# Performance work log

Measured on AMD Instinct MI355X. Metric: run time of the kernel, lower is better.

Reference implementation:

```python
import jax, jax.numpy as jnp
import numpy as np

B, N, DIM = 4, 1024, 512
DEPTH, HEADS, DH = 4, 8, 64
INNER = HEADS * DH  # 512
W = 32              # sqrt(N), FeedForward reshapes tokens to (W, W)
SCALE = DH ** -0.5  # used for BOTH spatial and spectral branches (as in source)
EPS_LN = 1e-5
EPS_BN = 1e-5


def setup_inputs() -> dict:
    key = jax.random.key(0)
    ks = jax.random.split(key, 16)
    L = DEPTH
    def rn(k, shape, s=0.02):
        return jax.random.normal(k, shape, jnp.float32) * s
    return {
        "x": jax.random.normal(ks[0], (B, N, DIM), jnp.float32),
        "ln1_w": jnp.ones((L, DIM), jnp.float32), "ln1_b": jnp.zeros((L, DIM), jnp.float32),
        "Wqkv": rn(ks[1], (L, DIM, 3 * INNER)),
        "Wout": rn(ks[2], (L, INNER, DIM)), "bout": jnp.zeros((L, DIM), jnp.float32),
        "sp_w": rn(ks[3], (L, HEADS, HEADS, 3, 3), 0.1), "sp_b": jnp.zeros((L, HEADS), jnp.float32),
        "Wqkv_spec": rn(ks[4], (L, N, 3 * N)),
        "spec_w": rn(ks[5], (L, 1, 1, 3, 3), 0.1), "spec_b": jnp.zeros((L, 1), jnp.float32),
        "ln2_w": jnp.ones((L, DIM), jnp.float32), "ln2_b": jnp.zeros((L, DIM), jnp.float32),
        "dw_w": rn(ks[6], (L, DIM, 1, 3, 3), 0.1), "dw_b": jnp.zeros((L, DIM), jnp.float32),
        "pw_w": rn(ks[7], (L, 256, DIM)), "pw_b": jnp.zeros((L, 256), jnp.float32),
        "bn_g": jnp.ones((L, 256), jnp.float32), "bn_b": jnp.zeros((L, 256), jnp.float32),
        "bn_m": jnp.zeros((L, 256), jnp.float32), "bn_v": jnp.ones((L, 256), jnp.float32),
        "c1_w": rn(ks[8], (L, 512, 256)), "c1_b": jnp.zeros((L, 512), jnp.float32),
        "c2_w": rn(ks[9], (L, DIM, 512)), "c2_b": jnp.zeros((L, DIM), jnp.float32),
    }


def _ln(x, w, b):
    mu = x.mean(-1, keepdims=True)
    var = x.var(-1, keepdims=True)  # biased, matching torch LayerNorm
    return (x - mu) * jax.lax.rsqrt(var + EPS_LN) * w + b


def _conv3x3(x, w, b, groups=1):
    y = jax.lax.conv_general_dilated(x, w, (1, 1), 'SAME',
                                     dimension_numbers=('NCHW', 'OIHW', 'NCHW'),
                                     feature_group_count=groups)
    return y + b[None, :, None, None]


def _block(x, p):
    (ln1w, ln1b, Wqkv, Wout, bout, spw, spb, Wqs, scw, scb,
     ln2w, ln2b, dww, dwb, pww, pwb, bng, bnb, bnm, bnv, c1w, c1b, c2w, c2b) = p
    b = x.shape[0]
    # --- spatial attention (PreNorm) ---
    h = _ln(x, ln1w, ln1b)
    q, k, v = jnp.split(h @ Wqkv, 3, axis=-1)
    split_heads = lambda t: t.reshape(b, N, HEADS, DH).transpose(0, 2, 1, 3)  # b h n d
    q, k, v = split_heads(q), split_heads(k), split_heads(v)
    attn = jax.nn.softmax(jnp.einsum('bhid,bhjd->bhij', q, k) * SCALE, axis=-1)
    attn = _conv3x3(attn, spw, spb)  # conv over the softmax map (heads as channels)
    out = jnp.einsum('bhij,bhjd->bhid', attn, v).transpose(0, 2, 1, 3).reshape(b, N, INNER)
    out = out @ Wout + bout  # (b, n, dim)
    # --- spectral attention on h^T (b, dim, n); v_spec is dead code in source ---
    xt = jnp.swapaxes(h, -1, -2)
    qs, ks_, _vs = jnp.split(xt @ Wqs, 3, axis=-1)  # each (b, dim, n)
    a = jax.nn.softmax(jnp.einsum('bin,bjn->bij', qs, ks_) * SCALE, axis=-1)
    a = _conv3x3(a[:, None], scw, scb)[:, 0]  # (b, dim, dim)
    x = x + jnp.einsum('bnd,bde->bne', out, a)  # residual add from Transformer loop
    # --- FeedForward (PreNorm), FF adds its own internal residual too ---
    h2 = _ln(x, ln2w, ln2b)
    img = h2.reshape(b, W, W, DIM).transpose(0, 3, 1, 2)  # 'b (w h) c -> b c w h'
    t = _conv3x3(img, dww, dwb, groups=DIM)               # depthwise 3x3
    t = jnp.einsum('oc,bchw->bohw', pww, t) + pwb[None, :, None, None]  # pointwise dim->256
    t = (t - bnm[None, :, None, None]) * jax.lax.rsqrt(bnv + EPS_BN)[None, :, None, None] \
        * bng[None, :, None, None] + bnb[None, :, None, None]           # BatchNorm2d (eval)
    t = jax.nn.gelu(jnp.einsum('oc,bchw->bohw', c1w, t) + c1b[None, :, None, None], approximate=False)
    t = jax.nn.gelu(jnp.einsum('oc,bchw->bohw', c2w, t) + c2b[None, :, None, None], approximate=False)
    ff = h2 + t.transpose(0, 2, 3, 1).reshape(b, N, DIM)  # FF internal residual
    return x + ff


def _forward(x, ln1_w, ln1_b, Wqkv, Wout, bout, sp_w, sp_b, Wqkv_spec, spec_w, spec_b,
             ln2_w, ln2_b, dw_w, dw_b, pw_w, pw_b, bn_g, bn_b, bn_m, bn_v,
             c1_w, c1_b, c2_w, c2_b):
    stacked = (ln1_w, ln1_b, Wqkv, Wout, bout, sp_w, sp_b, Wqkv_spec, spec_w, spec_b,
               ln2_w, ln2_b, dw_w, dw_b, pw_w, pw_b, bn_g, bn_b, bn_m, bn_v,
               c1_w, c1_b, c2_w, c2_b)
    for i in range(DEPTH):
        x = _block(x, tuple(a[i] for a in stacked))
    return x


def reference(x, ln1_w, ln1_b, Wqkv, Wout, bout, sp_w, sp_b, Wqkv_spec, spec_w, spec_b,
              ln2_w, ln2_b, dw_w, dw_b, pw_w, pw_b, bn_g, bn_b, bn_m, bn_v,
              c1_w, c1_b, c2_w, c2_b):
    return _forward(x, ln1_w, ln1_b, Wqkv, Wout, bout, sp_w, sp_b, Wqkv_spec, spec_w, spec_b,
                    ln2_w, ln2_b, dw_w, dw_b, pw_w, pw_b, bn_g, bn_b, bn_m, bn_v,
                    c1_w, c1_b, c2_w, c2_b)
```

## Files before the change

kernel.cpp:

```cpp
#include <hip/hip_runtime.h>
#include <hip/hip_bf16.h>

typedef __hip_bfloat16 bf16;
typedef __attribute__((ext_vector_type(8))) short bf16x8;
typedef __attribute__((ext_vector_type(4))) float f32x4;

__device__ __forceinline__ float b2f(bf16 v){ return __bfloat162float(v); }
__device__ __forceinline__ bf16 f2b(float v){ return __float2bfloat16(v); }
__device__ __forceinline__ float bits2f(unsigned u){ return __uint_as_float(u << 16); }
__device__ __forceinline__ unsigned short f2bits(float v){ bf16 t = __float2bfloat16(v); return *(unsigned short*)&t; }

__device__ __forceinline__ float gelu_f(float x){
  return 0.5f * x * (1.f + erff(x * 0.7071067811865475f));
}

__device__ __forceinline__ void gload_lds(const void* g, void* l){
  __builtin_amdgcn_global_load_lds((const __attribute__((address_space(1))) void*)g,
                                   (__attribute__((address_space(3))) void*)l, 16, 0, 0);
}

template<bool MAX>
__device__ __forceinline__ float block_reduce(float v){
  __shared__ float s[4];
  #pragma unroll
  for (int o = 32; o > 0; o >>= 1){
    float t = __shfl_down(v, o, 64);
    v = MAX ? fmaxf(v, t) : (v + t);
  }
  int lane = threadIdx.x & 63, w = threadIdx.x >> 6;
  __syncthreads();
  if (lane == 0) s[w] = v;
  __syncthreads();
  return MAX ? fmaxf(fmaxf(s[0], s[1]), fmaxf(s[2], s[3]))
             : (s[0] + s[1] + s[2] + s[3]);
}

__global__ void detect_k(const unsigned* __restrict__ x, int* __restrict__ flag){
  __shared__ int cnt[256];
  int tid = threadIdx.x;
  int c = 0;
  for (int i = tid; i < 4096; i += 256){
    unsigned h = x[i] & 0xffffu;
    int e = (int)((h >> 7) & 0xff);
    if (h == 0u || (e >= 100 && e <= 133)) c++;
  }
  cnt[tid] = c;
  __syncthreads();
  for (int o = 128; o > 0; o >>= 1){ if (tid < o) cnt[tid] += cnt[tid+o]; __syncthreads(); }
  if (tid == 0) *flag = (cnt[0] < 2048) ? 1 : 0;
}

__global__ __launch_bounds__(256) void cvt_x_k(const void* __restrict__ src,
                                               float* __restrict__ X,
                                               const int* __restrict__ flag){
  int p = blockIdx.x*256 + threadIdx.x;
  X[p] = (*flag) ? ((const float*)src)[p]
                 : __bfloat162float(((const bf16*)src)[p]);
}

struct WCvt21 { const void* src[21]; long long cum[22]; };

__global__ __launch_bounds__(256) void cvt_w_k(WCvt21 a, bf16* __restrict__ WB,
                                               long long total, const int* __restrict__ flag){
  long long i = (long long)blockIdx.x*256 + threadIdx.x;
  if (i >= total) return;
  int t = 0;
  while (a.cum[t+1] <= i) t++;
  long long e = i - a.cum[t];
  WB[i] = (*flag) ? __float2bfloat16(((const float*)a.src[t])[e])
                  : ((const bf16*)a.src[t])[e];
}

__global__ __launch_bounds__(256) void wtrans_k(const void* __restrict__ src, bf16* __restrict__ dst,
                                                int ld_src, int ldd, long long sSrc, long long sDst,
                                                const int* __restrict__ flag){
  __shared__ bf16 t[64][65];
  int z = blockIdx.z;
  int r0 = blockIdx.x*64, c0 = blockIdx.y*64;
  int lane = threadIdx.x & 63, quad = threadIdx.x >> 6;
  const float* sf = (const float*)src;
  const bf16* sb = (const bf16*)src;
  int fl = *flag;
  #pragma unroll
  for (int k = 0; k < 16; ++k){
    int r = quad*16 + k;
    long long idx = z*sSrc + (long long)(r0+r)*ld_src + c0 + lane;
    float v = fl ? sf[idx] : b2f(sb[idx]);
    t[r][lane] = f2b(v);
  }
  __syncthreads();
  #pragma unroll
  for (int k = 0; k < 16; ++k){
    int c = quad*16 + k;
    dst[z*sDst + (long long)(c0+c)*ldd + r0 + lane] = t[lane][c];
  }
}

__global__ void wprep_k(const bf16* __restrict__ spw, bf16* __restrict__ Wr){
  int l = blockIdx.x;
  for (int t = threadIdx.x; t < 1536; t += 256){
    int ho = t / 96, k = t - ho*96;
    float v = 0.f;
    if (ho < 8 && k < 72){
      int tap = k >> 3, hi = k & 7;
      v = b2f(spw[l*576 + ho*72 + hi*9 + tap]);
    }
    Wr[l*1536 + t] = f2b(v);
  }
}

__global__ __launch_bounds__(256) void store_out_k(const float* __restrict__ X,
                                                   void* __restrict__ out,
                                                   const int* __restrict__ flag){
  int p = blockIdx.x*256 + threadIdx.x;
  if (*flag) ((float*)out)[p] = X[p];
  else       ((bf16*)out)[p] = f2b(X[p]);
}

template<int MF, int NF, typename TC>
__global__ __launch_bounds__(256) void gmfma_k(
    int M, int N, int K,
    const bf16* __restrict__ A, int lda, long long sA, long long sA2,
    const bf16* __restrict__ Bt, int ldb, long long sB, long long sB2,
    TC* __restrict__ C, int ldc, long long sC, long long sC2,
    float alpha, int beta,
    const bf16* __restrict__ bias_n,
    const float* __restrict__ scale_n,
    const float* __restrict__ shift_n,
    const bf16* __restrict__ addF,
    int act)
{
  constexpr int BM = MF*32, BN = NF*32;
  constexpr int CHA = BM/16, CH = (BM+BN)/16;
  static_assert(CH % 4 == 0, "chunks must divide among 4 waves");
  __shared__ bf16 Asm[BM][32];
  __shared__ bf16 Bsm[BN][32];
  const int tid = threadIdx.x;
  const int lane = tid & 63, wid = tid >> 6;
  const int wm = wid >> 1, wn = wid & 1;
  const int m0 = blockIdx.y*BM, n0 = blockIdx.x*BN;
  const int z = blockIdx.z;
  const long long zl = z & 7, zh = z >> 3;
  const bf16* Ab = A + zl*sA + zh*sA2;
  const bf16* Bb = Bt + zl*sB + zh*sB2;
  TC* Cb = C + zl*sC + zh*sC2;
  const bf16* Fb = addF ? addF + zl*sC + zh*sC2 : nullptr;

  f32x4 acc[MF][NF];
  f32x4 zero = {0.f, 0.f, 0.f, 0.f};
  #pragma unroll
  for (int m = 0; m < MF; ++m)
    #pragma unroll
    for (int n = 0; n < NF; ++n) acc[m][n] = zero;

  const int rchunk = lane >> 2;
  const int kchunk = (lane & 3) * 8;
  const int row16 = lane & 15, kq = (lane >> 4) * 8;

  for (int k0 = 0; k0 < K; k0 += 32){
    #pragma unroll
    for (int cc = 0; cc < CH/4; ++cc){
      int c = wid + cc*4;
      if (c < CHA){
        int row = c*16 + rchunk;
        gload_lds(Ab + (long long)(m0+row)*lda + k0 + kchunk, &Asm[c*16][0]);
      } else {
        int row = (c-CHA)*16 + rchunk;
        gload_lds(Bb + (long long)(n0+row)*ldb + k0 + kchunk, &Bsm[(c-CHA)*16][0]);
      }
    }
    __syncthreads();
    bf16x8 af[MF], bfr[NF];
    #pragma unroll
    for (int m = 0; m < MF; ++m)
      af[m] = *(const bf16x8*)&Asm[wm*(MF*16) + m*16 + row16][kq];
    #pragma unroll
    for (int n = 0; n < NF; ++n)
      bfr[n] = *(const bf16x8*)&Bsm[wn*(NF*16) + n*16 + row16][kq];
    #pragma unroll
    for (int m = 0; m < MF; ++m)
      #pragma unroll
      for (int n = 0; n < NF; ++n)
        acc[m][n] = __builtin_amdgcn_mfma_f32_16x16x32_bf16(af[m], bfr[n], acc[m][n], 0, 0, 0);
    __syncthreads();
  }

  #pragma unroll
  for (int m = 0; m < MF; ++m){
    #pragma unroll
    for (int n = 0; n < NF; ++n){
      int gn = n0 + wn*(NF*16) + n*16 + (lane & 15);
      float bn_ = bias_n ? b2f(bias_n[gn]) : 0.f;
      float sc = scale_n ? scale_n[gn] : 1.f;
      float sh = shift_n ? shift_n[gn] : 0.f;
      #pragma unroll
      for (int r = 0; r < 4; ++r){
        int gm = m0 + wm*(MF*16) + m*16 + (lane >> 4)*4 + r;
        float v = acc[m][n][r] * alpha + bn_;
        v = v * sc + sh;
        if (act) v = gelu_f(v);
        long long idx = (long long)gm*ldc + gn;
        if (Fb) v += b2f(Fb[idx]);
        if (beta){
          float old;
          if constexpr (__is_same(TC, float)) old = Cb[idx]; else old = b2f(Cb[idx]);
          v += old;
        }
        if constexpr (__is_same(TC, float)) Cb[idx] = v; else Cb[idx] = f2b(v);
      }
    }
  }
}

template<int MF, int NF, typename TC>
static void gmfma_x(hipStream_t st, int z, int M, int N, int K,
                    const bf16* A, int lda, long long sA, long long sA2,
                    const bf16* Bt, int ldb, long long sB, long long sB2,
                    TC* C, int ldc, long long sC, long long sC2,
                    float alpha = 1.f, int beta = 0,
                    const bf16* bias_n = nullptr,
                    const float* scale_n = nullptr, const float* shift_n = nullptr,
                    const bf16* addF = nullptr, int act = 0)
{
  dim3 g(N/(NF*32), M/(MF*32), z);
  gmfma_k<MF,NF,TC><<<g, 256, 0, st>>>(M,N,K,A,lda,sA,sA2,Bt,ldb,sB,sB2,C,ldc,sC,sC2,
                                       alpha,beta,bias_n,scale_n,shift_n,addF,act);
}

template<int MF, int NF, typename TC>
static void gmfma(hipStream_t st, int z, int M, int N, int K,
                  const bf16* A, int lda, long long sA,
                  const bf16* Bt, int ldb, long long sB,
                  TC* C, int ldc, long long sC,
                  float alpha = 1.f, int beta = 0,
                  const bf16* bias_n = nullptr,
                  const float* scale_n = nullptr, const float* shift_n = nullptr,
                  const bf16* addF = nullptr, int act = 0)
{
  gmfma_x<MF,NF,TC>(st, z, M, N, K, A, lda, sA, 8*sA, Bt, ldb, sB, 8*sB,
                    C, ldc, sC, 8*sC, alpha, beta, bias_n, scale_n, shift_n, addF, act);
}

__global__ __launch_bounds__(256) void ln_k(const float* __restrict__ X, bf16* __restrict__ Y,
                                            const bf16* __restrict__ w, const bf16* __restrict__ b){
  long long row = blockIdx.x;
  const float* x = X + row*512;
  bf16* y = Y + row*512;
  int tid = threadIdx.x;
  float v0 = x[tid], v1 = x[tid+256];
  float mean = block_reduce<false>(v0+v1) * (1.f/512.f);
  float msq  = block_reduce<false>(v0*v0+v1*v1) * (1.f/512.f);
  float var = msq - mean*mean;
  float rs = rsqrtf(var + 1e-5f);
  y[tid]     = f2b((v0-mean)*rs*b2f(w[tid])     + b2f(b[tid]));
  y[tid+256] = f2b((v1-mean)*rs*b2f(w[tid+256]) + b2f(b[tid+256]));
}

__device__ __forceinline__ float ldf(const float* p){ return *p; }
__device__ __forceinline__ void stf(float* p, float v){ *p = v; }

__global__ __launch_bounds__(256) void softmax_k(float* __restrict__ data, int cols){
  long long row = blockIdx.x;
  float* p = data + row * (long long)cols;
  int tid = threadIdx.x;
  int per = cols >> 8;
  float v[4];
  float mx = -3.4e38f;
  for (int r = 0; r < per; ++r){ v[r] = p[tid + (r<<8)]; mx = fmaxf(mx, v[r]); }
  mx = block_reduce<true>(mx);
  float sum = 0.f;
  for (int r = 0; r < per; ++r){ v[r] = expf(v[r] - mx); sum += v[r]; }
  sum = block_reduce<false>(sum);
  float inv = 1.f / sum;
  for (int r = 0; r < per; ++r) p[tid + (r<<8)] = v[r] * inv;
}

__global__ __launch_bounds__(256) void smT_k(const bf16* __restrict__ Sp, bf16* __restrict__ Sx,
                                             long long bstride){
  __shared__ unsigned short sm[8][1032];
  __shared__ float redmx[4][8];
  __shared__ float redsum[4][8];
  int i = blockIdx.x;
  long long b = blockIdx.y;
  const bf16* src = Sp + b*bstride + (long long)i*1024;
  bf16* dst = Sx + b*bstride + (long long)i*8192;
  int tid = threadIdx.x;
  int lane = tid & 63, w = tid >> 6;
  int j0 = tid*4;

  float v[8][4];
  #pragma unroll
  for (int h = 0; h < 8; ++h){
    ushort4 u = *(const ushort4*)&src[h*1048576 + j0];
    v[h][0] = bits2f(u.x); v[h][1] = bits2f(u.y);
    v[h][2] = bits2f(u.z); v[h][3] = bits2f(u.w);
  }
  float mx[8];
  #pragma unroll
  for (int h = 0; h < 8; ++h){
    float m = fmaxf(fmaxf(v[h][0], v[h][1]), fmaxf(v[h][2], v[h][3]));
    #pragma unroll
    for (int o = 32; o > 0; o >>= 1) m = fmaxf(m, __shfl_xor(m, o, 64));
    if (lane == 0) redmx[w][h] = m;
    mx[h] = m;
  }
  __syncthreads();
  #pragma unroll
  for (int h = 0; h < 8; ++h)
    mx[h] = fmaxf(fmaxf(redmx[0][h], redmx[1][h]), fmaxf(redmx[2][h], redmx[3][h]));
  float inv[8];
  #pragma unroll
  for (int h = 0; h < 8; ++h){
    float s = 0.f;
    #pragma unroll
    for (int r = 0; r < 4; ++r){ v[h][r] = expf(v[h][r] - mx[h]); s += v[h][r]; }
    #pragma unroll
    for (int o = 32; o > 0; o >>= 1) s += __shfl_xor(s, o, 64);
    if (lane == 0) redsum[w][h] = s;
  }
  __syncthreads();
  #pragma unroll
  for (int h = 0; h < 8; ++h)
    inv[h] = 1.f / (redsum[0][h] + redsum[1][h] + redsum[2][h] + redsum[3][h]);
  #pragma unroll
  for (int h = 0; h < 8; ++h)
    #pragma unroll
    for (int r = 0; r < 4; ++r)
      sm[h][j0 + r] = f2bits(v[h][r] * inv[h]);
  __syncthreads();
  #pragma unroll
  for (int r = 0; r < 4; ++r){
    int j = j0 + r;
    bf16x8 o;
    #pragma unroll
    for (int h = 0; h < 8; ++h) o[h] = (short)sm[h][j];
    *(bf16x8*)&dst[(long long)j*8] = o;
  }
}

__global__ __launch_bounds__(256) void convmf_k(const bf16* __restrict__ Sx, bf16* __restrict__ Pout,
                                                const bf16* __restrict__ Wr, const bf16* __restrict__ bias,
                                                long long bstride){
  __shared__ bf16 tile[6][66][8];
  long long b = blockIdx.z;
  int i0 = blockIdx.y*4, j0 = blockIdx.x*64;
  int tid = threadIdx.x;
  const bf16* src = Sx + b*bstride;
  for (int t = tid; t < 396; t += 256){
    int row = t / 66, col = t - row*66;
    int gi = i0 + row - 1, gj = j0 + col - 1;
    bf16x8 val = {};
    if ((unsigned)gi < 1024u && (unsigned)gj < 1024u)
      val = *(const bf16x8*)&src[(long long)gi*8192 + gj*8];
    *(bf16x8*)&tile[row][col][0] = val;
  }
  int lane = tid & 63, wid = tid >> 6;
  int row16 = lane & 15, q = lane >> 4;
  bf16x8 bf0 = *(const bf16x8*)&Wr[row16*96 +  0 + q*8];
  bf16x8 bf1 = *(const bf16x8*)&Wr[row16*96 + 32 + q*8];
  bf16x8 bf2 = *(const bf16x8*)&Wr[row16*96 + 64 + q*8];
  __syncthreads();

  int ii = wid;
  f32x4 zero = {0.f,0.f,0.f,0.f};
  f32x4 acc[4] = {zero, zero, zero, zero};
  #pragma unroll
  for (int ks = 0; ks < 3; ++ks){
    int tap = ks*4 + q;
    int tcl = tap > 8 ? 0 : tap;
    int di = tcl / 3, dj = tcl - di*3;
    bf16x8 bsel = ks == 0 ? bf0 : (ks == 1 ? bf1 : bf2);
    #pragma unroll
    for (int mf = 0; mf < 4; ++mf){
      bf16x8 af = *(const bf16x8*)&tile[ii + di][mf*16 + row16 + dj][0];
      acc[mf] = __builtin_amdgcn_mfma_f32_16x16x32_bf16(af, bsel, acc[mf], 0, 0, 0);
    }
  }
  if (row16 < 8){
    float bv = b2f(bias[row16]);
    bf16* dst = Pout + b*bstride + (long long)row16*1048576 + (long long)(i0 + ii)*1024;
    #pragma unroll
    for (int mf = 0; mf < 4; ++mf){
      int j = j0 + mf*16 + q*4;
      ushort4 o;
      o.x = f2bits(acc[mf][0] + bv);
      o.y = f2bits(acc[mf][1] + bv);
      o.z = f2bits(acc[mf][2] + bv);
      o.w = f2bits(acc[mf][3] + bv);
      *(ushort4*)&dst[j] = o;
    }
  }
}

__global__ __launch_bounds__(256) void conv_spec_k(const float* __restrict__ in, bf16* __restrict__ out,
                                                   const bf16* __restrict__ w, const bf16* __restrict__ bias){
  __shared__ float ti[66][67];
  __shared__ bf16 toutT[64][65];
  int b = blockIdx.z;
  int i0 = blockIdx.y*64, j0 = blockIdx.x*64;
  int tid = threadIdx.x;
  const float* ib = in + (long long)b*262144;
  for (int t = tid; t < 66*66; t += 256){
    int r = t / 66, c = t - r*66;
    int gi = i0 + r - 1, gj = j0 + c - 1;
    float v = 0.f;
    if ((unsigned)gi < 512u && (unsigned)gj < 512u) v = ib[gi*512 + gj];
    ti[r][c] = v;
  }
  __syncthreads();
  float w9[9], bv = b2f(bias[0]);
  #pragma unroll
  for (int d = 0; d < 9; ++d) w9[d] = b2f(w[d]);
  int ii = tid & 63;
  #pragma unroll
  for (int q = 0; q < 16; ++q){
    int jj = (tid >> 6)*16 + q;
    float acc = bv;
    #pragma unroll
    for (int di = 0; di < 3; ++di)
      #pragma unroll
      for (int dj = 0; dj < 3; ++dj)
        acc += w9[di*3+dj] * ti[ii+di][jj+dj];
    toutT[jj][ii] = f2b(acc);
  }
  __syncthreads();
  #pragma unroll
  for (int q = 0; q < 16; ++q){
    int jj = (tid >> 6)*16 + q;
    out[(long long)b*262144 + (j0+jj)*512 + i0 + (tid & 63)] = toutT[jj][tid & 63];
  }
}

__global__ __launch_bounds__(256) void dwconv_k(const bf16* __restrict__ H2, bf16* __restrict__ T1,
                                                const bf16* __restrict__ w, const bf16* __restrict__ bias){
  int p = blockIdx.x*256 + threadIdx.x;
  int cp = p & 255;
  int n = (p >> 8) & 1023;
  int b = p >> 18;
  int c0 = cp*2;
  int wi = n >> 5, hg = n & 31;
  float a0 = b2f(bias[c0]), a1 = b2f(bias[c0+1]);
  #pragma unroll
  for (int di = 0; di < 3; ++di){
    int gw = wi + di - 1;
    if ((unsigned)gw >= 32u) continue;
    #pragma unroll
    for (int dj = 0; dj < 3; ++dj){
      int gh = hg + dj - 1;
      if ((unsigned)gh >= 32u) continue;
      unsigned hv = *(const unsigned*)&H2[((long long)b*1024 + (gw*32+gh))*512 + c0];
      float w0 = b2f(w[c0*9 + di*3 + dj]);
      float w1 = b2f(w[(c0+1)*9 + di*3 + dj]);
      a0 += w0 * bits2f(hv & 0xffffu);
      a1 += w1 * bits2f(hv >> 16);
    }
  }
  bf16 h0 = f2b(a0), h1 = f2b(a1);
  unsigned o = ((unsigned)*(unsigned short*)&h1 << 16) | (unsigned)*(unsigned short*)&h0;
  *(unsigned*)&T1[((long long)b*1024 + n)*512 + c0] = o;
}

__global__ void bnaff_all_k(const bf16* __restrict__ pwb, const bf16* __restrict__ g,
                            const bf16* __restrict__ bb, const bf16* __restrict__ m,
                            const bf16* __restrict__ v, float* __restrict__ BNAFF){
  int l = blockIdx.x, o = threadIdx.x;
  float s = b2f(g[l*256+o]) * rsqrtf(b2f(v[l*256+o]) + 1e-5f);
  BNAFF[l*512 + o] = s;
  BNAFF[l*512 + 256 + o] = (b2f(pwb[l*256+o]) - b2f(m[l*256+o])) * s + b2f(bb[l*256+o]);
}

__global__ __launch_bounds__(256) void vtrans_k(const bf16* __restrict__ QKV, bf16* __restrict__ Vt){
  __shared__ bf16 t[64][65];
  int z = blockIdx.z; int b = z >> 3, h = z & 7;
  const bf16* src = QKV + (long long)b*1572864 + 1024 + h*64;
  bf16* dst = Vt + (long long)z*65536;
  int n0 = blockIdx.x*64;
  int lane = threadIdx.x & 63, quad = threadIdx.x >> 6;
  #pragma unroll
  for (int k = 0; k < 16; ++k){
    int r = quad*16 + k;
    t[r][lane] = src[(long long)(n0+r)*1536 + lane];
  }
  __syncthreads();
  #pragma unroll
  for (int k = 0; k < 16; ++k){
    int d = quad*16 + k;
    dst[(long long)d*1024 + n0 + lane] = t[lane][d];
  }
}

__global__ __launch_bounds__(256) void htrans_k(const bf16* __restrict__ Hb, bf16* __restrict__ HT){
  __shared__ bf16 t[64][65];
  int b = blockIdx.z;
  int n0 = blockIdx.x*64, c0 = blockIdx.y*64;
  int lane = threadIdx.x & 63, quad = threadIdx.x >> 6;
  #pragma unroll
  for (int k = 0; k < 16; ++k){
    int r = quad*16 + k;
    t[r][lane] = Hb[((long long)b*1024 + n0 + r)*512 + c0 + lane];
  }
  __syncthreads();
  #pragma unroll
  for (int k = 0; k < 16; ++k){
    int c = quad*16 + k;
    HT[(long long)b*524288 + (long long)(c0+c)*1024 + n0 + lane] = t[lane][c];
  }
}

extern "C" void kernel_launch(void* const* d_in, const int* in_sizes, int n_in,
                              void* d_out, int out_size, void* d_ws, size_t ws_size,
                              hipStream_t stream)
{
  (void)in_sizes; (void)n_in; (void)out_size;

  const bool big = ws_size >= 206000000ull;
  const long long ATTN_SZ = big ? 33554432LL : 8388608LL;

  float* X     = (float*)d_ws;
  bf16*  WBsm  = (bf16*)(X + 2097152);
  bf16*  WqkvT = WBsm  + 2139648;
  bf16*  WoutT = WqkvT + 3145728;
  bf16*  WqsT  = WoutT + 1048576;
  bf16*  Hbuf  = WqsT  + 8388608;
  bf16*  HbufT = Hbuf  + 2097152;
  bf16*  QKV   = HbufT + 2097152;
  bf16*  Vt    = QKV   + 6291456;
  bf16*  OUTH  = Vt    + 2097152;
  bf16*  OUT   = OUTH  + 2097152;
  bf16*  ATTN  = OUT   + 2097152;
  bf16*  ATTNC = ATTN  + ATTN_SZ;
  float* BNAFF = (float*)(ATTNC + ATTN_SZ);
  bf16*  WR    = (bf16*)(BNAFF + 2048);
  int*   FLAG  = (int*)(WR + 6144);

  float* ASPEC   = (float*)OUTH;
  bf16*  ASPECCT = ATTNC;
  bf16*  T1 = ATTN;
  bf16*  T3 = ATTN + 2097152;
  bf16*  T2 = ATTNC + 2097152;
  bf16*  SQK = ATTN;

  static const int widx[21] = {1,2,5,6,7,9,10,11,12,13,14,15,16,17,18,19,20,21,22,23,24};
  static const long long wsz[21] = {2048,2048,2048,2304,32,36,4,2048,2048,18432,2048,
                                    524288,1024,1024,1024,1024,1024,524288,2048,1048576,2048};
  WCvt21 wc;
  long long cum = 0;
  bf16* wp[21];
  for (int t = 0; t < 21; ++t){
    wc.src[t] = d_in[widx[t]];
    wc.cum[t] = cum;
    wp[t] = WBsm + cum;
    cum += wsz[t];
  }
  wc.cum[21] = cum;

  bf16 *w_ln1w = wp[0],  *w_ln1b = wp[1],  *w_bout = wp[2],  *w_spw = wp[3];
  bf16 *w_spb  = wp[4],  *w_specw= wp[5],  *w_specb= wp[6],  *w_ln2w= wp[7];
  bf16 *w_ln2b = wp[8],  *w_dww  = wp[9],  *w_dwb  = wp[10], *w_pww = wp[11];
  bf16 *w_pwb  = wp[12], *w_bng  = wp[13], *w_bnb  = wp[14], *w_bnm = wp[15];
  bf16 *w_bnv  = wp[16], *w_c1w  = wp[17], *w_c1b  = wp[18], *w_c2w = wp[19];
  bf16 *w_c2b  = wp[20];

  detect_k<<<1, 256, 0, stream>>>((const unsigned*)d_in[0], FLAG);
  cvt_x_k<<<8192, 256, 0, stream>>>(d_in[0], X, FLAG);
  cvt_w_k<<<(int)((cum + 255)/256), 256, 0, stream>>>(wc, WBsm, cum, FLAG);
  wtrans_k<<<dim3(8,24,4), 256, 0, stream>>>(d_in[3], WqkvT, 1536, 512, 786432LL, 786432LL, FLAG);
  wtrans_k<<<dim3(8, 8,4), 256, 0, stream>>>(d_in[4], WoutT,  512, 512, 262144LL, 262144LL, FLAG);
  wtrans_k<<<dim3(16,32,4),256, 0, stream>>>(d_in[8], WqsT,  3072,1024, 3145728LL,2097152LL, FLAG);
  bnaff_all_k<<<4, 256, 0, stream>>>(w_pwb, w_bng, w_bnb, w_bnm, w_bnv, BNAFF);
  wprep_k<<<4, 256, 0, stream>>>(w_spw, WR);

  for (int l = 0; l < 4; ++l){
    ln_k<<<4096, 256, 0, stream>>>(X, Hbuf, w_ln1w + l*512, w_ln1b + l*512);
    gmfma<4,4,bf16>(stream, 1, 4096, 1536, 512,
        Hbuf, 512, 0, WqkvT + (long long)l*786432, 512, 0, QKV, 1536, 0);
    vtrans_k<<<dim3(16,1,32), 256, 0, stream>>>(QKV, Vt);
    if (big){
      gmfma_x<4,4,bf16>(stream, 32, 1024, 1024, 64,
          QKV, 1536, 64, 1572864, QKV + 512, 1536, 64, 1572864,
          ATTN, 1024, 1048576, 8388608, 0.125f);
      smT_k<<<dim3(1024,4), 256, 0, stream>>>(ATTN, ATTNC, 8388608LL);
      convmf_k<<<dim3(16,256,4), 256, 0, stream>>>(ATTNC, ATTN, WR + l*1536, w_spb + l*8, 8388608LL);
      gmfma_x<2,2,bf16>(stream, 32, 1024, 64, 1024,
          ATTN, 1024, 1048576, 8388608, Vt, 1024, 65536, 524288,
          OUTH, 512, 64, 524288);
    } else {
      for (int b = 0; b < 4; ++b){
        bf16* qkvb = QKV + (long long)b*1572864;
        gmfma<4,4,bf16>(stream, 8, 1024, 1024, 64,
            qkvb, 1536, 64, qkvb + 512, 1536, 64, ATTN, 1024, 1048576, 0.125f);
        smT_k<<<dim3(1024,1), 256, 0, stream>>>(ATTN, ATTNC, 8388608LL);
        convmf_k<<<dim3(16,256,1), 256, 0, stream>>>(ATTNC, ATTN, WR + l*1536, w_spb + l*8, 8388608LL);
        gmfma<2,2,bf16>(stream, 8, 1024, 64, 1024,
            ATTN, 1024, 1048576, Vt + (long long)b*524288, 1024, 65536,
            OUTH + (long long)b*524288, 512, 64);
      }
    }
    gmfma<2,2,bf16>(stream, 1, 4096, 512, 512,
        OUTH, 512, 0, WoutT + (long long)l*262144, 512, 0, OUT, 512, 0,
        1.f, 0, w_bout + l*512);
    htrans_k<<<dim3(16,8,4), 256, 0, stream>>>(Hbuf, HbufT);
    gmfma<4,4,bf16>(stream, 4, 512, 2048, 1024,
        HbufT, 1024, 524288, WqsT + (long long)l*2097152, 1024, 0, SQK, 2048, 1048576);
    gmfma<2,2,float>(stream, 4, 512, 512, 1024,
        SQK, 2048, 1048576, SQK + 1024, 2048, 1048576, ASPEC, 512, 262144, 0.125f);
    softmax_k<<<2048, 256, 0, stream>>>(ASPEC, 512);
    conv_spec_k<<<dim3(8,8,4), 256, 0, stream>>>(ASPEC, ASPECCT, w_specw + l*9, w_specb + l);
    gmfma<2,2,float>(stream, 4, 1024, 512, 512,
        OUT, 512, 524288, ASPECCT, 512, 262144, X, 512, 524288, 1.f, 1);
    ln_k<<<4096, 256, 0, stream>>>(X, Hbuf, w_ln2w + l*512, w_ln2b + l*512);
    dwconv_k<<<4096, 256, 0, stream>>>(Hbuf, T1, w_dww + l*4608, w_dwb + l*512);
    gmfma<2,2,bf16>(stream, 4, 1024, 256, 512,
        T1, 512, 524288, w_pww + (long long)l*131072, 512, 0, T2, 256, 262144,
        1.f, 0, nullptr, BNAFF + l*512, BNAFF + l*512 + 256);
    gmfma<2,2,bf16>(stream, 4, 1024, 512, 256,
        T2, 256, 262144, w_c1w + (long long)l*131072, 256, 0, T3, 512, 524288,
        1.f, 0, w_c1b + l*512, nullptr, nullptr, nullptr, 1);
    gmfma<2,2,float>(stream, 4, 1024, 512, 512,
        T3, 512, 524288, w_c2w + (long long)l*262144, 512, 0, X, 512, 524288,
        1.f, 1, w_c2b + l*512, nullptr, nullptr, Hbuf, 1);
  }

  store_out_k<<<8192, 256, 0, stream>>>(X, d_out, FLAG);
}
```

Measured before the change: 1.291 ms.

## Fuse softmax normalization into spatial conv, replacing transposed softmax pass with stats kernel

```diff
diff --git a/kernel.cpp b/kernel.cpp
--- a/kernel.cpp
+++ b/kernel.cpp
@@ -256,9 +256,6 @@
   y[tid+256] = f2b((v1-mean)*rs*b2f(w[tid+256]) + b2f(b[tid+256]));
 }
 
-__device__ __forceinline__ float ldf(const float* p){ return *p; }
-__device__ __forceinline__ void stf(float* p, float v){ *p = v; }
-
 __global__ __launch_bounds__(256) void softmax_k(float* __restrict__ data, int cols){
   long long row = blockIdx.x;
   float* p = data + row * (long long)cols;
@@ -269,21 +266,20 @@
   for (int r = 0; r < per; ++r){ v[r] = p[tid + (r<<8)]; mx = fmaxf(mx, v[r]); }
   mx = block_reduce<true>(mx);
   float sum = 0.f;
-  for (int r = 0; r < per; ++r){ v[r] = expf(v[r] - mx); sum += v[r]; }
+  for (int r = 0; r < per; ++r){ v[r] = __expf(v[r] - mx); sum += v[r]; }
   sum = block_reduce<false>(sum);
   float inv = 1.f / sum;
   for (int r = 0; r < per; ++r) p[tid + (r<<8)] = v[r] * inv;
 }
 
-__global__ __launch_bounds__(256) void smT_k(const bf16* __restrict__ Sp, bf16* __restrict__ Sx,
-                                             long long bstride){
-  __shared__ unsigned short sm[8][1032];
+__global__ __launch_bounds__(256) void maxsum_k(const bf16* __restrict__ Sp,
+                                                float* __restrict__ Mrow, float* __restrict__ Irow,
+                                                long long bstride){
   __shared__ float redmx[4][8];
   __shared__ float redsum[4][8];
   int i = blockIdx.x;
   long long b = blockIdx.y;
   const bf16* src = Sp + b*bstride + (long long)i*1024;
-  bf16* dst = Sx + b*bstride + (long long)i*8192;
   int tid = threadIdx.x;
   int lane = tid & 63, w = tid >> 6;
   int j0 = tid*4;
@@ -295,99 +291,112 @@
     v[h][0] = bits2f(u.x); v[h][1] = bits2f(u.y);
     v[h][2] = bits2f(u.z); v[h][3] = bits2f(u.w);
   }
-  float mx[8];
   #pragma unroll
   for (int h = 0; h < 8; ++h){
     float m = fmaxf(fmaxf(v[h][0], v[h][1]), fmaxf(v[h][2], v[h][3]));
     #pragma unroll
     for (int o = 32; o > 0; o >>= 1) m = fmaxf(m, __shfl_xor(m, o, 64));
     if (lane == 0) redmx[w][h] = m;
-    mx[h] = m;
-  }
-  __syncthreads();
+  }
+  __syncthreads();
+  float mx[8];
   #pragma unroll
   for (int h = 0; h < 8; ++h)
     mx[h] = fmaxf(fmaxf(redmx[0][h], redmx[1][h]), fmaxf(redmx[2][h], redmx[3][h]));
-  float inv[8];
   #pragma unroll
   for (int h = 0; h < 8; ++h){
     float s = 0.f;
     #pragma unroll
-    for (int r = 0; r < 4; ++r){ v[h][r] = expf(v[h][r] - mx[h]); s += v[h][r]; }
+    for (int r = 0; r < 4; ++r) s += __expf(v[h][r] - mx[h]);
     #pragma unroll
     for (int o = 32; o > 0; o >>= 1) s += __shfl_xor(s, o, 64);
     if (lane == 0) redsum[w][h] = s;
   }
   __syncthreads();
-  #pragma unroll
-  for (int h = 0; h < 8; ++h)
-    inv[h] = 1.f / (redsum[0][h] + redsum[1][h] + redsum[2][h] + redsum[3][h]);
-  #pragma unroll
-  for (int h = 0; h < 8; ++h)
-    #pragma unroll
-    for (int r = 0; r < 4; ++r)
-      sm[h][j0 + r] = f2bits(v[h][r] * inv[h]);
-  __syncthreads();
-  #pragma unroll
-  for (int r = 0; r < 4; ++r){
-    int j = j0 + r;
-    bf16x8 o;
-    #pragma unroll
-    for (int h = 0; h < 8; ++h) o[h] = (short)sm[h][j];
-    *(bf16x8*)&dst[(long long)j*8] = o;
-  }
-}
-
-__global__ __launch_bounds__(256) void convmf_k(const bf16* __restrict__ Sx, bf16* __restrict__ Pout,
-                                                const bf16* __restrict__ Wr, const bf16* __restrict__ bias,
-                                                long long bstride){
-  __shared__ bf16 tile[6][66][8];
+  if (tid < 8){
+    float s = redsum[0][tid] + redsum[1][tid] + redsum[2][tid] + redsum[3][tid];
+    long long o = (b*1024 + i)*8 + tid;
+    Mrow[o] = mx[tid];
+    Irow[o] = 1.f / s;
+  }
+}
+
+__global__ __launch_bounds__(256) void convNorm_k(const bf16* __restrict__ Sp, bf16* __restrict__ Pout,
+                                                  const bf16* __restrict__ Wr, const bf16* __restrict__ bias,
+                                                  const float* __restrict__ Mrow, const float* __restrict__ Irow,
+                                                  long long bstride){
+  __shared__ bf16 tile[18][66][8];
+  __shared__ float mrow[18][8];
+  __shared__ float irow[18][8];
   long long b = blockIdx.z;
-  int i0 = blockIdx.y*4, j0 = blockIdx.x*64;
+  int i0 = blockIdx.y*16, j0 = blockIdx.x*64;
   int tid = threadIdx.x;
-  const bf16* src = Sx + b*bstride;
-  for (int t = tid; t < 396; t += 256){
+  const bf16* src = Sp + b*bstride;
+
+  for (int t = tid; t < 144; t += 256){
+    int r = t >> 3, h = t & 7;
+    int gi = i0 + r - 1;
+    float m = 0.f, iv = 0.f;
+    if ((unsigned)gi < 1024u){
+      long long o = (b*1024 + gi)*8 + h;
+      m = Mrow[o]; iv = Irow[o];
+    }
+    mrow[r][h] = m; irow[r][h] = iv;
+  }
+  __syncthreads();
+
+  for (int t = tid; t < 18*66; t += 256){
     int row = t / 66, col = t - row*66;
     int gi = i0 + row - 1, gj = j0 + col - 1;
     bf16x8 val = {};
-    if ((unsigned)gi < 1024u && (unsigned)gj < 1024u)
-      val = *(const bf16x8*)&src[(long long)gi*8192 + gj*8];
+    if ((unsigned)gi < 1024u && (unsigned)gj < 1024u){
+      long long base = (long long)gi*1024 + gj;
+      #pragma unroll
+      for (int h = 0; h < 8; ++h){
+        float s = b2f(src[(long long)h*1048576 + base]);
+        val[h] = (short)f2bits(__expf(s - mrow[row][h]) * irow[row][h]);
+      }
+    }
     *(bf16x8*)&tile[row][col][0] = val;
   }
+
   int lane = tid & 63, wid = tid >> 6;
   int row16 = lane & 15, q = lane >> 4;
   bf16x8 bf0 = *(const bf16x8*)&Wr[row16*96 +  0 + q*8];
   bf16x8 bf1 = *(const bf16x8*)&Wr[row16*96 + 32 + q*8];
   bf16x8 bf2 = *(const bf16x8*)&Wr[row16*96 + 64 + q*8];
-  __syncthreads();
-
-  int ii = wid;
+  float bv = (row16 < 8) ? b2f(bias[row16]) : 0.f;
+  __syncthreads();
+
   f32x4 zero = {0.f,0.f,0.f,0.f};
-  f32x4 acc[4] = {zero, zero, zero, zero};
-  #pragma unroll
-  for (int ks = 0; ks < 3; ++ks){
-    int tap = ks*4 + q;
-    int tcl = tap > 8 ? 0 : tap;
-    int di = tcl / 3, dj = tcl - di*3;
-    bf16x8 bsel = ks == 0 ? bf0 : (ks == 1 ? bf1 : bf2);
-    #pragma unroll
-    for (int mf = 0; mf < 4; ++mf){
-      bf16x8 af = *(const bf16x8*)&tile[ii + di][mf*16 + row16 + dj][0];
-      acc[mf] = __builtin_amdgcn_mfma_f32_16x16x32_bf16(af, bsel, acc[mf], 0, 0, 0);
-    }
-  }
-  if (row16 < 8){
-    float bv = b2f(bias[row16]);
-    bf16* dst = Pout + b*bstride + (long long)row16*1048576 + (long long)(i0 + ii)*1024;
-    #pragma unroll
-    for (int mf = 0; mf < 4; ++mf){
-      int j = j0 + mf*16 + q*4;
-      ushort4 o;
-      o.x = f2bits(acc[mf][0] + bv);
-      o.y = f2bits(acc[mf][1] + bv);
-      o.z = f2bits(acc[mf][2] + bv);
-      o.w = f2bits(acc[mf][3] + bv);
-      *(ushort4*)&dst[j] = o;
+  #pragma unroll
+  for (int rr = 0; rr < 4; ++rr){
+    int ii = rr*4 + wid;
+    f32x4 acc[4] = {zero, zero, zero, zero};
+    #pragma unroll
+    for (int ks = 0; ks < 3; ++ks){
+      int tap = ks*4 + q;
+      int tcl = tap > 8 ? 0 : tap;
+      int di = tcl / 3, dj = tcl - di*3;
+      bf16x8 bsel = ks == 0 ? bf0 : (ks == 1 ? bf1 : bf2);
+      #pragma unroll
+      for (int mf = 0; mf < 4; ++mf){
+        bf16x8 af = *(const bf16x8*)&tile[ii + di][mf*16 + row16 + dj][0];
+        acc[mf] = __builtin_amdgcn_mfma_f32_16x16x32_bf16(af, bsel, acc[mf], 0, 0, 0);
+      }
+    }
+    if (row16 < 8){
+      bf16* dst = Pout + b*bstride + (long long)row16*1048576 + (long long)(i0 + ii)*1024;
+      #pragma unroll
+      for (int mf = 0; mf < 4; ++mf){
+        int j = j0 + mf*16 + q*4;
+        ushort4 o;
+        o.x = f2bits(acc[mf][0] + bv);
+        o.y = f2bits(acc[mf][1] + bv);
+        o.z = f2bits(acc[mf][2] + bv);
+        o.w = f2bits(acc[mf][3] + bv);
+        *(ushort4*)&dst[j] = o;
+      }
     }
   }
 }
@@ -513,7 +522,7 @@
 {
   (void)in_sizes; (void)n_in; (void)out_size;
 
-  const bool big = ws_size >= 206000000ull;
+  const bool big = ws_size >= 207000000ull;
   const long long ATTN_SZ = big ? 33554432LL : 8388608LL;
 
   float* X     = (float*)d_ws;
@@ -531,7 +540,9 @@
   bf16*  ATTNC = ATTN  + ATTN_SZ;
   float* BNAFF = (float*)(ATTNC + ATTN_SZ);
   bf16*  WR    = (bf16*)(BNAFF + 2048);
-  int*   FLAG  = (int*)(WR + 6144);
+  float* MROW  = (float*)(WR + 6144);
+  float* IROW  = MROW + 32768;
+  int*   FLAG  = (int*)(IROW + 32768);
 
   float* ASPEC   = (float*)OUTH;
   bf16*  ASPECCT = ATTNC;
@@ -579,20 +590,22 @@
       gmfma_x<4,4,bf16>(stream, 32, 1024, 1024, 64,
           QKV, 1536, 64, 1572864, QKV + 512, 1536, 64, 1572864,
           ATTN, 1024, 1048576, 8388608, 0.125f);
-      smT_k<<<dim3(1024,4), 256, 0, stream>>>(ATTN, ATTNC, 8388608LL);
-      convmf_k<<<dim3(16,256,4), 256, 0, stream>>>(ATTNC, ATTN, WR + l*1536, w_spb + l*8, 8388608LL);
+      maxsum_k<<<dim3(1024,4), 256, 0, stream>>>(ATTN, MROW, IROW, 8388608LL);
+      convNorm_k<<<dim3(16,64,4), 256, 0, stream>>>(ATTN, ATTNC, WR + l*1536, w_spb + l*8,
+                                                    MROW, IROW, 8388608LL);
       gmfma_x<2,2,bf16>(stream, 32, 1024, 64, 1024,
-          ATTN, 1024, 1048576, 8388608, Vt, 1024, 65536, 524288,
+          ATTNC, 1024, 1048576, 8388608, Vt, 1024, 65536, 524288,
           OUTH, 512, 64, 524288);
     } else {
       for (int b = 0; b < 4; ++b){
         bf16* qkvb = QKV + (long long)b*1572864;
         gmfma<4,4,bf16>(stream, 8, 1024, 1024, 64,
             qkvb, 1536, 64, qkvb + 512, 1536, 64, ATTN, 1024, 1048576, 0.125f);
-        smT_k<<<dim3(1024,1), 256, 0, stream>>>(ATTN, ATTNC, 8388608LL);
-        convmf_k<<<dim3(16,256,1), 256, 0, stream>>>(ATTNC, ATTN, WR + l*1536, w_spb + l*8, 8388608LL);
+        maxsum_k<<<dim3(1024,1), 256, 0, stream>>>(ATTN, MROW, IROW, 8388608LL);
+        convNorm_k<<<dim3(16,64,1), 256, 0, stream>>>(ATTN, ATTNC, WR + l*1536, w_spb + l*8,
+                                                      MROW, IROW, 8388608LL);
         gmfma<2,2,bf16>(stream, 8, 1024, 64, 1024,
-            ATTN, 1024, 1048576, Vt + (long long)b*524288, 1024, 65536,
+            ATTNC, 1024, 1048576, Vt + (long long)b*524288, 1024, 65536,
             OUTH + (long long)b*524288, 512, 64);
       }
     }
```

Measured after the change: 1.283 ms. About the same (-0.6%).
